# Performance work log

Hardware: AMD Instinct MI355X
Metric: run time of the kernel (lower is better)

Reference implementation:

```python
import jax, jax.numpy as jnp
import numpy as np

NUM_COMPONENTS = 32
RESOLUTION = 512
NUM_POINTS = 2_000_000


def setup_inputs() -> dict:
    key = jax.random.key(0)
    kp, k0, k1, k2 = jax.random.split(key, 4)
    # positions are grid_sample-style normalized coords in [-1, 1]
    positions = jax.random.uniform(kp, (NUM_POINTS, 3), jnp.float32, -1.0, 1.0)
    vec_x = jax.random.normal(k0, (NUM_COMPONENTS, RESOLUTION), jnp.float32)
    vec_y = jax.random.normal(k1, (NUM_COMPONENTS, RESOLUTION), jnp.float32)
    vec_z = jax.random.normal(k2, (NUM_COMPONENTS, RESOLUTION), jnp.float32)
    return {"positions": positions, "vec_x": vec_x, "vec_y": vec_y, "vec_z": vec_z}


def _sample_1d(vec, x):
    """1D bilinear lookup mimicking grid_sample(align_corners=True, padding='zeros').
    vec: [C, R] per-axis CP vectors; x: [N] coords in [-1, 1]. Returns [C, N]."""
    R = vec.shape[1]
    ix = (x + 1.0) * 0.5 * (R - 1)          # map [-1,1] -> [0, R-1]
    i0 = jnp.floor(ix)
    w1 = ix - i0                              # right-neighbor weight
    i0i = i0.astype(jnp.int32)
    i1i = i0i + 1

    def gather(idx):
        valid = (idx >= 0) & (idx < R)        # zero-padding outside the grid
        g = jnp.take(vec, jnp.clip(idx, 0, R - 1), axis=1)  # [C, N]
        return jnp.where(valid[None, :], g, 0.0)

    return gather(i0i) * (1.0 - w1)[None, :] + gather(i1i) * w1[None, :]


def reference(positions, vec_x, vec_y, vec_z):
    # positions: [..., 3]; unbind per axis, 1D-sample each CP vector set, product-reduce.
    batch_shape = positions.shape[:-1]
    flat = positions.reshape(-1, 3)
    fx = _sample_1d(vec_x, flat[:, 0])  # [C, N]
    fy = _sample_1d(vec_y, flat[:, 1])  # [C, N]
    fz = _sample_1d(vec_z, flat[:, 2])  # [C, N]
    feats = fx * fy * fz                 # elementwise product over axes, [C, N]
    return feats.T.reshape(*batch_shape, vec_x.shape[0])  # [..., C]
```

## Files before the change

### kernel.cpp

```cpp
#include <hip/hip_runtime.h>

#define NC 32
#define NR 512
#define HC 16
#define NCHUNK 256
#define BLK 1024

#define LDS_FLOATS (3 * NR * HC + HC)
#define LDS_BYTES (LDS_FLOATS * 4)

__global__ __launch_bounds__(256) void transpose_vecs(
    const float* __restrict__ vx, const float* __restrict__ vy,
    const float* __restrict__ vz, float* __restrict__ tx,
    float* __restrict__ ty, float* __restrict__ tz) {
  int u = blockIdx.x * 256 + threadIdx.x;
  if (u >= 3 * NC * NR) return;
  int table = u >> 14;
  int e = u & (NC * NR - 1);
  int c = e >> 9;
  int r = e & (NR - 1);
  const float* src = (table == 0) ? vx : (table == 1) ? vy : vz;
  float* dst = (table == 0) ? tx : (table == 1) ? ty : tz;
  dst[((c >> 4) << 13) + (r << 4) + (c & (HC - 1))] = src[e];
}

__device__ __forceinline__ float4 lerp4(const float* __restrict__ t,
                                        float x, int j4) {
  float ix = fmaf(x, 0.5f * (NR - 1), 0.5f * (NR - 1));
  ix = fminf(fmaxf(ix, 0.0f), (float)(NR - 1));
  float f = floorf(ix);
  float w = ix - f;
  int i0 = (int)f;
  const float* a = t + (i0 << 4) + j4;
  float4 v0 = *(const float4*)a;
  float4 v1 = *(const float4*)(a + HC);
  float4 r;
  r.x = fmaf(w, v1.x - v0.x, v0.x);
  r.y = fmaf(w, v1.y - v0.y, v0.y);
  r.z = fmaf(w, v1.z - v0.z, v0.z);
  r.w = fmaf(w, v1.w - v0.w, v0.w);
  return r;
}

__global__ __launch_bounds__(BLK) void cp_encode_lds(
    const float* __restrict__ pos, const float* __restrict__ tx,
    const float* __restrict__ ty, const float* __restrict__ tz,
    float* __restrict__ out, int npts, int chunk_pts) {
  extern __shared__ float lds[];
  int tid = threadIdx.x;
  int base_p = blockIdx.x * chunk_pts;
  int pend = min(base_p + chunk_pts, npts);
  int iters = (chunk_pts + (BLK / 4) - 1) >> 8;

  int j4 = (tid & 3) << 2;
  int pofs = tid >> 2;

  for (int h = 0; h < 2; ++h) {
    __syncthreads();
    for (int u = tid; u < 3 * NR * 4; u += BLK) {
      int a = u >> 11;
      int rem = u & 2047;
      const float* src = (a == 0) ? tx : (a == 1) ? ty : tz;
      float4 v = *(const float4*)(src + (h << 13) + (rem << 2));
      *(float4*)(&lds[(a << 13) + (rem << 2)]) = v;
    }
    if (h == 0 && tid < HC) lds[3 * NR * HC + tid] = 0.0f;
    __syncthreads();

    int p = base_p + pofs;
    int pc = min(p, npts - 1);
    float x = pos[3 * pc], y = pos[3 * pc + 1], z = pos[3 * pc + 2];

    for (int it = 0; it < iters; ++it) {
      int pn = p + (BLK / 4);
      float xn = 0.f, yn = 0.f, zn = 0.f;
      if (it + 1 < iters) {
        int pcn = min(pn, npts - 1);
        xn = pos[3 * pcn];
        yn = pos[3 * pcn + 1];
        zn = pos[3 * pcn + 2];
      }
      float4 fx = lerp4(lds, x, j4);
      float4 fy = lerp4(lds + (NR * HC), y, j4);
      float4 fz = lerp4(lds + 2 * (NR * HC), z, j4);
      float4 r;
      r.x = fx.x * fy.x * fz.x;
      r.y = fx.y * fy.y * fz.y;
      r.z = fx.z * fy.z * fz.z;
      r.w = fx.w * fy.w * fz.w;
      if (p < pend)
        *(float4*)(out + (size_t)p * NC + h * HC + j4) = r;
      p = pn; x = xn; y = yn; z = zn;
    }
  }
}

__device__ __forceinline__ float4 sample4_u(const float* __restrict__ t,
                                            float x, int c4) {
  float ix = (x + 1.0f) * 0.5f * (float)(NR - 1);
  float f = floorf(ix);
  float w = ix - f;
  int i0 = (int)f;
  int i1 = i0 + 1;
  float m0 = (i0 >= 0 && i0 < NR) ? (1.0f - w) : 0.0f;
  float m1 = (i1 >= 0 && i1 < NR) ? w : 0.0f;
  int ci0 = min(max(i0, 0), NR - 1);
  int ci1 = min(max(i1, 0), NR - 1);
  float4 r;
  float* rp = (float*)&r;
  for (int j = 0; j < 4; ++j) {
    float v0 = t[(c4 + j) * NR + ci0];
    float v1 = t[(c4 + j) * NR + ci1];
    rp[j] = v0 * m0 + v1 * m1;
  }
  return r;
}

__global__ __launch_bounds__(256) void cp_encode_global(
    const float* __restrict__ pos, const float* __restrict__ vx,
    const float* __restrict__ vy, const float* __restrict__ vz,
    float* __restrict__ out, int npts) {
  int t = blockIdx.x * 256 + threadIdx.x;
  int p = t >> 3;
  if (p >= npts) return;
  int c4 = (t & 7) * 4;
  float x = pos[3 * p + 0];
  float y = pos[3 * p + 1];
  float z = pos[3 * p + 2];
  float4 fx = sample4_u(vx, x, c4);
  float4 fy = sample4_u(vy, y, c4);
  float4 fz = sample4_u(vz, z, c4);
  float4 r;
  r.x = fx.x * fy.x * fz.x;
  r.y = fx.y * fy.y * fz.y;
  r.z = fx.z * fy.z * fz.z;
  r.w = fx.w * fy.w * fz.w;
  *(float4*)(out + (long long)p * NC + c4) = r;
}

extern "C" void kernel_launch(void* const* d_in, const int* in_sizes, int n_in,
                              void* d_out, int out_size, void* d_ws,
                              size_t ws_size, hipStream_t stream) {
  const float* pos = (const float*)d_in[0];
  const float* vx = (const float*)d_in[1];
  const float* vy = (const float*)d_in[2];
  const float* vz = (const float*)d_in[3];
  float* out = (float*)d_out;
  int npts = in_sizes[0] / 3;

  const size_t tbytes = (size_t)3 * NC * NR * sizeof(float);

  if (ws_size >= tbytes) {
    static int lds_attr_set = 0;
    if (!lds_attr_set) {
      hipFuncSetAttribute((const void*)cp_encode_lds,
                          hipFuncAttributeMaxDynamicSharedMemorySize,
                          LDS_BYTES);
      lds_attr_set = 1;
    }
    float* tx = (float*)d_ws;
    float* ty = tx + NC * NR;
    float* tz = ty + NC * NR;
    int tb = (3 * NC * NR + 255) / 256;
    transpose_vecs<<<tb, 256, 0, stream>>>(vx, vy, vz, tx, ty, tz);
    int chunk_pts = (npts + NCHUNK - 1) / NCHUNK;
    cp_encode_lds<<<NCHUNK, BLK, LDS_BYTES, stream>>>(pos, tx, ty, tz, out,
                                                      npts, chunk_pts);
  } else {
    int blocks = (npts * 8 + 255) / 256;
    cp_encode_global<<<blocks, 256, 0, stream>>>(pos, vx, vy, vz, out, npts);
  }
}
```

Measured before the change: 357.8 us.

## Launch many small blocks with register-held points and combined half-channel stores

Replaces the fixed 256 large chunks with one block per 1024 points. Each thread loads four points' coordinates into registers up front and keeps the first half-channel results in registers, so both halves of a point are written together after the second LDS table pass. The change targets poor latency hiding and strided half-row writes. The cost is that every block reloads the 96KB LDS table twice for only 1024 points, which greatly increases table-staging traffic relative to compute. It also clamps the floor index to avoid reading a padding slot.

```diff
diff --git a/kernel.cpp b/kernel.cpp
--- a/kernel.cpp
+++ b/kernel.cpp
@@ -3,10 +3,11 @@
 #define NC 32
 #define NR 512
 #define HC 16
-#define NCHUNK 256
 #define BLK 1024
+#define PPB 1024
+#define ITERS 4
 
-#define LDS_FLOATS (3 * NR * HC + HC)
+#define LDS_FLOATS (3 * NR * HC)
 #define LDS_BYTES (LDS_FLOATS * 4)
 
 __global__ __launch_bounds__(256) void transpose_vecs(
@@ -28,7 +29,7 @@
                                         float x, int j4) {
   float ix = fmaf(x, 0.5f * (NR - 1), 0.5f * (NR - 1));
   ix = fminf(fmaxf(ix, 0.0f), (float)(NR - 1));
-  float f = floorf(ix);
+  float f = fminf(floorf(ix), (float)(NR - 2));
   float w = ix - f;
   int i0 = (int)f;
   const float* a = t + (i0 << 4) + j4;
@@ -42,18 +43,26 @@
   return r;
 }
 
-__global__ __launch_bounds__(BLK) void cp_encode_lds(
+__global__ __launch_bounds__(BLK, 4) void cp_encode_lds(
     const float* __restrict__ pos, const float* __restrict__ tx,
     const float* __restrict__ ty, const float* __restrict__ tz,
-    float* __restrict__ out, int npts, int chunk_pts) {
+    float* __restrict__ out, int npts) {
   extern __shared__ float lds[];
   int tid = threadIdx.x;
-  int base_p = blockIdx.x * chunk_pts;
-  int pend = min(base_p + chunk_pts, npts);
-  int iters = (chunk_pts + (BLK / 4) - 1) >> 8;
-
+  int base_p = blockIdx.x * PPB;
   int j4 = (tid & 3) << 2;
   int pofs = tid >> 2;
+
+  float xs[ITERS], ys[ITERS], zs[ITERS];
+  float4 r0[ITERS];
+#pragma unroll
+  for (int it = 0; it < ITERS; ++it) {
+    int p = base_p + pofs + it * (BLK / 4);
+    int pc = min(p, npts - 1);
+    xs[it] = pos[3 * pc + 0];
+    ys[it] = pos[3 * pc + 1];
+    zs[it] = pos[3 * pc + 2];
+  }
 
   for (int h = 0; h < 2; ++h) {
     __syncthreads();
@@ -61,36 +70,31 @@
       int a = u >> 11;
       int rem = u & 2047;
       const float* src = (a == 0) ? tx : (a == 1) ? ty : tz;
-      float4 v = *(const float4*)(src + (h << 13) + (rem << 2));
-      *(float4*)(&lds[(a << 13) + (rem << 2)]) = v;
+      *(float4*)(&lds[(a << 13) + (rem << 2)]) =
+          *(const float4*)(src + (h << 13) + (rem << 2));
     }
-    if (h == 0 && tid < HC) lds[3 * NR * HC + tid] = 0.0f;
     __syncthreads();
 
-    int p = base_p + pofs;
-    int pc = min(p, npts - 1);
-    float x = pos[3 * pc], y = pos[3 * pc + 1], z = pos[3 * pc + 2];
-
-    for (int it = 0; it < iters; ++it) {
-      int pn = p + (BLK / 4);
-      float xn = 0.f, yn = 0.f, zn = 0.f;
-      if (it + 1 < iters) {
-        int pcn = min(pn, npts - 1);
-        xn = pos[3 * pcn];
-        yn = pos[3 * pcn + 1];
-        zn = pos[3 * pcn + 2];
-      }
-      float4 fx = lerp4(lds, x, j4);
-      float4 fy = lerp4(lds + (NR * HC), y, j4);
-      float4 fz = lerp4(lds + 2 * (NR * HC), z, j4);
+#pragma unroll
+    for (int it = 0; it < ITERS; ++it) {
+      float4 fx = lerp4(lds, xs[it], j4);
+      float4 fy = lerp4(lds + (NR * HC), ys[it], j4);
+      float4 fz = lerp4(lds + 2 * (NR * HC), zs[it], j4);
       float4 r;
       r.x = fx.x * fy.x * fz.x;
       r.y = fx.y * fy.y * fz.y;
       r.z = fx.z * fy.z * fz.z;
       r.w = fx.w * fy.w * fz.w;
-      if (p < pend)
-        *(float4*)(out + (size_t)p * NC + h * HC + j4) = r;
-      p = pn; x = xn; y = yn; z = zn;
+      if (h == 0) {
+        r0[it] = r;
+      } else {
+        int p = base_p + pofs + it * (BLK / 4);
+        if (p < npts) {
+          float* o = out + (size_t)p * NC;
+          *(float4*)(o + j4) = r0[it];
+          *(float4*)(o + HC + j4) = r;
+        }
+      }
     }
   }
 }
@@ -163,9 +167,9 @@
     float* tz = ty + NC * NR;
     int tb = (3 * NC * NR + 255) / 256;
     transpose_vecs<<<tb, 256, 0, stream>>>(vx, vy, vz, tx, ty, tz);
-    int chunk_pts = (npts + NCHUNK - 1) / NCHUNK;
-    cp_encode_lds<<<NCHUNK, BLK, LDS_BYTES, stream>>>(pos, tx, ty, tz, out,
-                                                      npts, chunk_pts);
+    int blocks = (npts + PPB - 1) / PPB;
+    cp_encode_lds<<<blocks, BLK, LDS_BYTES, stream>>>(pos, tx, ty, tz, out,
+                                                      npts);
   } else {
     int blocks = (npts * 8 + 255) / 256;
     cp_encode_global<<<blocks, 256, 0, stream>>>(pos, vx, vy, vz, out, npts);
```

Measured after the change: 318.2 us. -11.1%, faster.
